# Optimization experiments

Hardware: AMD Instinct MI355X
Metric: run time of the kernel (lower is better)

## Reference

```python
import jax, jax.numpy as jnp
import numpy as np

B, C, H, W = 8, 384, 32, 32
NUM_HEADS = 8
HEAD_DIM = C // NUM_HEADS


def setup_inputs() -> dict:
    key = jax.random.key(0)
    k1, k2, k3, k4, k5 = jax.random.split(key, 5)
    s = 1.0 / np.sqrt(C)
    return {
        "x": jax.random.normal(k1, (B, C, H, W), dtype=jnp.float32),
        "w_qkv": jax.random.normal(k2, (3 * C, C), dtype=jnp.float32) * s,   # 1x1 conv == linear over channels
        "b_qkv": jax.random.normal(k3, (3 * C,), dtype=jnp.float32) * 0.01,
        "w_proj": jax.random.normal(k4, (C, C), dtype=jnp.float32) * s,
        "b_proj": jax.random.normal(k5, (C,), dtype=jnp.float32) * 0.01,
    }


def reference(x, w_qkv, b_qkv, w_proj, b_proj):
    b, c, h, w = x.shape
    n = h * w
    scale = HEAD_DIM ** (-0.5)
    # 1x1 conv qkv: (B, 3C, H, W)
    qkv = jnp.einsum('bchw,oc->bohw', x, w_qkv) + b_qkv[None, :, None, None]
    # 'b (three hd d) h0 w0 -> three b hd (h0 w0) d'
    qkv = qkv.reshape(b, 3, NUM_HEADS, HEAD_DIM, n)
    qkv = jnp.transpose(qkv, (1, 0, 2, 4, 3))  # (3, B, heads, N, d)
    q, k, v = qkv[0], qkv[1], qkv[2]
    attn = jnp.einsum('bhnd,bhmd->bhnm', q, k) * scale
    attn = jax.nn.softmax(attn, axis=-1)
    out = jnp.einsum('bhnm,bhmd->bhnd', attn, v)          # (B, heads, N, d)
    out = jnp.transpose(out, (0, 1, 3, 2)).reshape(b, c, h, w)  # b (hd d) h w
    out = jnp.einsum('bchw,oc->bohw', out, w_proj) + b_proj[None, :, None, None]
    return out
```

## Files before the change

### kernel.cpp

```cpp
#include <hip/hip_runtime.h>
#include <hip/hip_bf16.h>

typedef __hip_bfloat16 bf16;
typedef __bf16 bfx8 __attribute__((ext_vector_type(8)));
typedef float f32x4 __attribute__((ext_vector_type(4)));

#define Bk   8
#define Ck   384
#define NHk  8
#define Dk   48
#define Dp   64
#define Nk   1024
#define O3   1152


__global__ __launch_bounds__(256) void xpose_kernel(
    const float* __restrict__ x, bf16* __restrict__ Xs)
{
    __shared__ bf16 tile[32][33];
    const int b = blockIdx.z, c0 = blockIdx.y * 32, n0 = blockIdx.x * 32;
    const int tn = threadIdx.x & 31, tc = threadIdx.x >> 5;
    const float* xb = x + (size_t)b * Ck * Nk;
    #pragma unroll
    for (int i = 0; i < 4; ++i)
        tile[tc + 8 * i][tn] = __float2bfloat16(xb[(size_t)(c0 + tc + 8 * i) * Nk + n0 + tn]);
    __syncthreads();
    bf16* base = Xs + ((size_t)b * 64 + (n0 >> 4)) * 48 * 128 + (c0 >> 3) * 128;
    #pragma unroll
    for (int i = 0; i < 4; ++i) {
        int n_loc = tc + 8 * i, c_loc = tn;
        base[(size_t)(n_loc >> 4) * 6144 + (c_loc >> 3) * 128 +
             (n_loc & 15) * 8 + (c_loc & 7)] = tile[c_loc][n_loc];
    }
}

__global__ __launch_bounds__(256) void wconv_kernel(
    const float* __restrict__ wq, const float* __restrict__ wp,
    bf16* __restrict__ Wq, bf16* __restrict__ Wp,
    bf16* __restrict__ Qs, bf16* __restrict__ Ks)
{
    int i = blockIdx.x * 256 + threadIdx.x;
    if (i < O3 * Ck) {
        int o = i / Ck, c = i - o * Ck;
        Wq[((size_t)(o >> 4) * 48 + (c >> 3)) * 128 + (o & 15) * 8 + (c & 7)] =
            __float2bfloat16(wq[i]);
    }
    if (i < Ck * Ck) {
        int o = i / Ck, c = i - o * Ck;
        Wp[((size_t)(o >> 4) * 48 + (c >> 3)) * 128 + (o & 15) * 8 + (c & 7)] =
            __float2bfloat16(wp[i]);
    }
    if (i < 262144) {
        int buf = i >> 17;
        int r17 = i & 131071;
        int head = r17 >> 11;
        int r11 = r17 & 2047;
        int g = r11 >> 5, c5 = r11 & 31;
        int cd = 6 + (c5 >> 4), e = c5 & 15;
        bf16* p = (buf ? Ks : Qs) + (size_t)head * 65536 +
                  ((size_t)g * 8 + cd) * 128 + e * 8;
        *(int4*)p = (int4){0, 0, 0, 0};
    }
}

__global__ __launch_bounds__(256) void qkv_mfma_kernel(
    const bf16* __restrict__ Xs, const bf16* __restrict__ Wq,
    const float* __restrict__ bias,
    bf16* __restrict__ Qs, bf16* __restrict__ Ks, bf16* __restrict__ Vs)
{
    const int b    = blockIdx.z;
    const int by   = blockIdx.y;
    const int bx   = blockIdx.x;
    const int o0   = by * 64;
    const int n0   = bx * 128;
    const int wave = threadIdx.x >> 6;
    const int lane = threadIdx.x & 63;
    const int l15  = lane & 15, quad = lane >> 4;
    const int t3   = o0 / Ck;

    const bf16* xg[2];
    const bf16* wg[4];
    #pragma unroll
    for (int i = 0; i < 2; ++i)
        xg[i] = Xs + ((size_t)(b * 64 + bx * 8 + wave * 2 + i) * 48) * 128 + lane * 8;
    #pragma unroll
    for (int j = 0; j < 4; ++j)
        wg[j] = Wq + ((size_t)(by * 4 + j) * 48) * 128 + lane * 8;

    f32x4 acc[8];
    #pragma unroll
    for (int i = 0; i < 8; ++i) acc[i] = (f32x4){0.f, 0.f, 0.f, 0.f};

    if (t3 < 2) {
        #pragma unroll
        for (int s = 0; s < 12; ++s) {
            bfx8 fx[2], fw[4];
            #pragma unroll
            for (int i = 0; i < 2; ++i) fx[i] = *(const bfx8*)(xg[i] + s * 512);
            #pragma unroll
            for (int j = 0; j < 4; ++j) fw[j] = *(const bfx8*)(wg[j] + s * 512);
            #pragma unroll
            for (int i = 0; i < 2; ++i)
                #pragma unroll
                for (int j = 0; j < 4; ++j)
                    acc[i * 4 + j] = __builtin_amdgcn_mfma_f32_16x16x32_bf16(
                        fx[i], fw[j], acc[i * 4 + j], 0, 0, 0);
        }
        const float qscale = 0.2082350964f;
        #pragma unroll
        for (int j = 0; j < 4; ++j) {
            int o  = o0 + j * 16 + l15;
            float bi = bias[o];
            int r  = o - t3 * Ck;
            int hd = r / Dk, d = r - hd * Dk;
            bf16* hb = (t3 == 0 ? Qs : Ks) + (size_t)(b * NHk + hd) * 65536
                     + (d >> 3) * 128 + (d & 7);
            #pragma unroll
            for (int i = 0; i < 2; ++i) {
                #pragma unroll
                for (int reg = 0; reg < 4; ++reg) {
                    int npos = n0 + wave * 32 + i * 16 + quad * 4 + reg;
                    float v = acc[i * 4 + j][reg] + bi;
                    if (t3 == 0) v *= qscale;
                    hb[(size_t)(npos >> 4) * 1024 + (npos & 15) * 8] = __float2bfloat16(v);
                }
            }
        }
    } else {
        #pragma unroll
        for (int s = 0; s < 12; ++s) {
            bfx8 fx[2], fw[4];
            #pragma unroll
            for (int i = 0; i < 2; ++i) fx[i] = *(const bfx8*)(xg[i] + s * 512);
            #pragma unroll
            for (int j = 0; j < 4; ++j) fw[j] = *(const bfx8*)(wg[j] + s * 512);
            #pragma unroll
            for (int j = 0; j < 4; ++j)
                #pragma unroll
                for (int i = 0; i < 2; ++i)
                    acc[j * 2 + i] = __builtin_amdgcn_mfma_f32_16x16x32_bf16(
                        fw[j], fx[i], acc[j * 2 + i], 0, 0, 0);
        }
        #pragma unroll
        for (int j = 0; j < 4; ++j) {
            #pragma unroll
            for (int reg = 0; reg < 4; ++reg) {
                int o  = o0 + j * 16 + quad * 4 + reg;
                float bi = bias[o];
                int r  = o - 2 * Ck;
                int hd = r / Dk, d = r - hd * Dk;
                bf16* vb = Vs + (size_t)(b * NHk + hd) * 49152
                         + ((size_t)(d >> 4) * 128) * 128 + (d & 15) * 8;
                #pragma unroll
                for (int i = 0; i < 2; ++i) {
                    int npos = n0 + wave * 32 + i * 16 + l15;
                    vb[(size_t)(npos >> 3) * 128 + (npos & 7)] =
                        __float2bfloat16(acc[j * 2 + i][reg] + bi);
                }
            }
        }
    }
}

__global__ __launch_bounds__(256) void attn_kernel(
    const bf16* __restrict__ Qs, const bf16* __restrict__ Ks,
    const bf16* __restrict__ Vs, bf16* __restrict__ AO)
{
    __shared__ __align__(16) short Ps[4 * 16 * 72];
    __shared__ float sums[4][16];

    const int bx   = blockIdx.x;
    const int hd   = blockIdx.y;
    const int b    = blockIdx.z;
    const int t    = threadIdx.x;
    const int wave = t >> 6;
    const int lane = t & 63;
    const int l15  = lane & 15;
    const int quad = lane >> 4;
    const int grp  = bx * 4 + wave;

    const bf16* qb = Qs + (size_t)(b * NHk + hd) * 65536;
    const bf16* kb = Ks + (size_t)(b * NHk + hd) * 65536;
    const bf16* vb = Vs + (size_t)(b * NHk + hd) * 49152;

    const bf16* qp = qb + ((size_t)grp * 8 + quad) * 128 + l15 * 8;
    const bfx8 bq0 = *(const bfx8*)(qp);
    const bfx8 bq1 = *(const bfx8*)(qp + 512);

    float l_run = 0.f;
    f32x4 oacc[3];
    #pragma unroll
    for (int dc = 0; dc < 3; ++dc) oacc[dc] = (f32x4){0.f, 0.f, 0.f, 0.f};

    short* PsW = Ps + wave * 16 * 72;

    for (int k0 = 0; k0 < Nk; k0 += 64) {
        f32x4 sf[4];
        #pragma unroll
        for (int s = 0; s < 4; ++s) {
            const bf16* kp = kb + ((size_t)((k0 >> 4) + s) * 8 + quad) * 128 + l15 * 8;
            const bfx8 kf0 = *(const bfx8*)(kp);
            const bfx8 kf1 = *(const bfx8*)(kp + 512);
            f32x4 z = (f32x4){0.f, 0.f, 0.f, 0.f};
            z = __builtin_amdgcn_mfma_f32_16x16x32_bf16(kf0, bq0, z, 0, 0, 0);
            z = __builtin_amdgcn_mfma_f32_16x16x32_bf16(kf1, bq1, z, 0, 0, 0);
            sf[s] = z;
        }

        float lsum = 0.f;
        #pragma unroll
        for (int s = 0; s < 4; ++s) {
            ushort4 pk;
            float e0 = __builtin_amdgcn_exp2f(sf[s][0]);
            float e1 = __builtin_amdgcn_exp2f(sf[s][1]);
            float e2 = __builtin_amdgcn_exp2f(sf[s][2]);
            float e3 = __builtin_amdgcn_exp2f(sf[s][3]);
            lsum += (e0 + e1) + (e2 + e3);
            bf16 h0 = __float2bfloat16(e0), h1 = __float2bfloat16(e1);
            bf16 h2 = __float2bfloat16(e2), h3 = __float2bfloat16(e3);
            pk.x = *(unsigned short*)&h0; pk.y = *(unsigned short*)&h1;
            pk.z = *(unsigned short*)&h2; pk.w = *(unsigned short*)&h3;
            *(ushort4*)&PsW[l15 * 72 + s * 16 + quad * 4] = pk;
        }
        l_run += lsum;

        asm volatile("s_waitcnt lgkmcnt(0)" ::: "memory");

        const bfx8 ap0 = *(const bfx8*)&PsW[l15 * 72 + quad * 8];
        const bfx8 ap1 = *(const bfx8*)&PsW[l15 * 72 + 32 + quad * 8];
        #pragma unroll
        for (int dc = 0; dc < 3; ++dc) {
            const bf16* vp = vb + ((size_t)dc * 128 + (k0 >> 3) + quad) * 128 + l15 * 8;
            const bfx8 bv0 = *(const bfx8*)(vp);
            const bfx8 bv1 = *(const bfx8*)(vp + 512);
            oacc[dc] = __builtin_amdgcn_mfma_f32_16x16x32_bf16(ap0, bv0, oacc[dc], 0, 0, 0);
            oacc[dc] = __builtin_amdgcn_mfma_f32_16x16x32_bf16(ap1, bv1, oacc[dc], 0, 0, 0);
        }
    }

    {
        float lt = l_run;
        lt += __shfl_xor(lt, 16, 64);
        lt += __shfl_xor(lt, 32, 64);
        sums[wave][l15] = lt;
    }
    asm volatile("s_waitcnt lgkmcnt(0)" ::: "memory");

    short* OsW = PsW;
    #pragma unroll
    for (int r = 0; r < 4; ++r) {
        int qi = quad * 4 + r;
        float rli = 1.0f / sums[wave][qi];
        #pragma unroll
        for (int dcc = 0; dcc < 3; ++dcc) {
            bf16 hb = __float2bfloat16(oacc[dcc][r] * rli);
            OsW[qi * 64 + dcc * 16 + l15] = *(short*)&hb;
        }
    }
    asm volatile("s_waitcnt lgkmcnt(0)" ::: "memory");

    bf16* aob = AO + (((size_t)b * 64 + grp) * 48 + hd * 6) * 128;
    {
        int u = lane;
        int4 v = *(const int4*)&OsW[(u & 15) * 64 + (u >> 4) * 8];
        *(int4*)(aob + u * 8) = v;
        if (lane < 32) {
            int u2 = 64 + lane;
            int4 v2 = *(const int4*)&OsW[(u2 & 15) * 64 + (u2 >> 4) * 8];
            *(int4*)(aob + u2 * 8) = v2;
        }
    }
}

__global__ __launch_bounds__(256) void proj_mfma_kernel(
    const bf16* __restrict__ AO, const bf16* __restrict__ Wp,
    const float* __restrict__ bias, float* __restrict__ out)
{
    const int b    = blockIdx.z;
    const int by   = blockIdx.y;
    const int bx   = blockIdx.x;
    const int o0   = by * 64;
    const int n0   = bx * 128;
    const int wave = threadIdx.x >> 6;
    const int lane = threadIdx.x & 63;
    const int l15  = lane & 15, quad = lane >> 4;

    const bf16* ag[2];
    const bf16* wg[4];
    #pragma unroll
    for (int i = 0; i < 2; ++i)
        ag[i] = AO + ((size_t)(b * 64 + bx * 8 + wave * 2 + i) * 48) * 128 + lane * 8;
    #pragma unroll
    for (int j = 0; j < 4; ++j)
        wg[j] = Wp + ((size_t)(by * 4 + j) * 48) * 128 + lane * 8;

    f32x4 acc[8];
    #pragma unroll
    for (int i = 0; i < 8; ++i) acc[i] = (f32x4){0.f, 0.f, 0.f, 0.f};

    #pragma unroll
    for (int s = 0; s < 12; ++s) {
        bfx8 fx[2], fw[4];
        #pragma unroll
        for (int i = 0; i < 2; ++i) fx[i] = *(const bfx8*)(ag[i] + s * 512);
        #pragma unroll
        for (int j = 0; j < 4; ++j) fw[j] = *(const bfx8*)(wg[j] + s * 512);
        #pragma unroll
        for (int j = 0; j < 4; ++j)
            #pragma unroll
            for (int i = 0; i < 2; ++i)
                acc[j * 2 + i] = __builtin_amdgcn_mfma_f32_16x16x32_bf16(
                    fw[j], fx[i], acc[j * 2 + i], 0, 0, 0);
    }

    #pragma unroll
    for (int j = 0; j < 4; ++j) {
        #pragma unroll
        for (int reg = 0; reg < 4; ++reg) {
            int o  = o0 + j * 16 + quad * 4 + reg;
            float bi = bias[o];
            #pragma unroll
            for (int i = 0; i < 2; ++i) {
                int npos = n0 + wave * 32 + i * 16 + l15;
                out[((size_t)b * Ck + o) * Nk + npos] = acc[j * 2 + i][reg] + bi;
            }
        }
    }
}

extern "C" void kernel_launch(void* const* d_in, const int* in_sizes, int n_in,
                              void* d_out, int out_size, void* d_ws, size_t ws_size,
                              hipStream_t stream)
{
    const float* x      = (const float*)d_in[0];
    const float* w_qkv  = (const float*)d_in[1];
    const float* b_qkv  = (const float*)d_in[2];
    const float* w_proj = (const float*)d_in[3];
    const float* b_proj = (const float*)d_in[4];
    float* out = (float*)d_out;

    const size_t XT_SEG = (size_t)Bk * Nk * Ck;
    const size_t WQ_SEG = (size_t)O3 * Ck;
    const size_t WP_SEG = (size_t)Ck * Ck;
    const size_t QK_SEG = (size_t)Bk * NHk * Nk * Dp;
    const size_t V_SEG  = (size_t)Bk * NHk * Dk * Nk;

    bf16* Xs = (bf16*)d_ws;
    bf16* Wq = Xs + XT_SEG;
    bf16* Wp = Wq + WQ_SEG;
    bf16* Qs = Wp + WP_SEG;
    bf16* Ks = Qs + QK_SEG;
    bf16* Vs = Ks + QK_SEG;
    bf16* AO = Vs + V_SEG;

    xpose_kernel<<<dim3(Nk / 32, Ck / 32, Bk), 256, 0, stream>>>(x, Xs);
    wconv_kernel<<<(O3 * Ck + 255) / 256, 256, 0, stream>>>(
        w_qkv, w_proj, Wq, Wp, Qs, Ks);
    qkv_mfma_kernel<<<dim3(Nk / 128, O3 / 64, Bk), 256, 0, stream>>>(
        Xs, Wq, b_qkv, Qs, Ks, Vs);
    attn_kernel<<<dim3(16, NHk, Bk), 256, 0, stream>>>(Qs, Ks, Vs, AO);
    proj_mfma_kernel<<<dim3(Nk / 128, Ck / 64, Bk), 256, 0, stream>>>(
        AO, Wp, b_proj, out);
}
```

Measured before the change: 134.3 us.

## Stage K and V tiles in shared memory per block in attention loop

Each iteration now cooperatively loads the 64-key K tile and the matching V tile into padded LDS buffers, bracketed by two __syncthreads. The four waves then read their MFMA operands from LDS instead of each fetching the same K/V fragments from global memory. This cuts redundant global/L2 traffic four-fold, at the cost of two block-wide barriers per iteration with no double buffering, so load latency is no longer hidden behind compute.

New measurement: 135.4 us. No clear change (+0.8%).

```diff
diff --git a/kernel.cpp b/kernel.cpp
--- a/kernel.cpp
+++ b/kernel.cpp
@@ -166,6 +166,8 @@
     const bf16* __restrict__ Qs, const bf16* __restrict__ Ks,
     const bf16* __restrict__ Vs, bf16* __restrict__ AO)
 {
+    __shared__ __align__(16) short Kls[32 * 136];
+    __shared__ __align__(16) short Vls[24 * 136];
     __shared__ __align__(16) short Ps[4 * 16 * 72];
     __shared__ float sums[4][16];
 
@@ -195,12 +197,35 @@
     short* PsW = Ps + wave * 16 * 72;
 
     for (int k0 = 0; k0 < Nk; k0 += 64) {
+        __syncthreads();
+        {
+            const bf16* ksrc = kb + (size_t)(k0 >> 4) * 1024;
+            #pragma unroll
+            for (int i = 0; i < 2; ++i) {
+                int u = t + 256 * i;
+                *(bfx8*)&Kls[(u >> 4) * 136 + (u & 15) * 8] =
+                    *(const bfx8*)(ksrc + u * 8);
+            }
+            {
+                int u = t;
+                *(bfx8*)&Vls[(u >> 4) * 136 + (u & 15) * 8] =
+                    *(const bfx8*)(vb + (size_t)(u >> 7) * 16384 +
+                                   (size_t)(k0 >> 3) * 128 + (u & 127) * 8);
+                if (t < 128) {
+                    int u2 = 256 + t;
+                    *(bfx8*)&Vls[(u2 >> 4) * 136 + (u2 & 15) * 8] =
+                        *(const bfx8*)(vb + (size_t)(u2 >> 7) * 16384 +
+                                       (size_t)(k0 >> 3) * 128 + (u2 & 127) * 8);
+                }
+            }
+        }
+        __syncthreads();
+
         f32x4 sf[4];
         #pragma unroll
         for (int s = 0; s < 4; ++s) {
-            const bf16* kp = kb + ((size_t)((k0 >> 4) + s) * 8 + quad) * 128 + l15 * 8;
-            const bfx8 kf0 = *(const bfx8*)(kp);
-            const bfx8 kf1 = *(const bfx8*)(kp + 512);
+            const bfx8 kf0 = *(const bfx8*)&Kls[(s * 8 + quad) * 136 + l15 * 8];
+            const bfx8 kf1 = *(const bfx8*)&Kls[(s * 8 + quad + 4) * 136 + l15 * 8];
             f32x4 z = (f32x4){0.f, 0.f, 0.f, 0.f};
             z = __builtin_amdgcn_mfma_f32_16x16x32_bf16(kf0, bq0, z, 0, 0, 0);
             z = __builtin_amdgcn_mfma_f32_16x16x32_bf16(kf1, bq1, z, 0, 0, 0);
@@ -230,9 +255,8 @@
         const bfx8 ap1 = *(const bfx8*)&PsW[l15 * 72 + 32 + quad * 8];
         #pragma unroll
         for (int dc = 0; dc < 3; ++dc) {
-            const bf16* vp = vb + ((size_t)dc * 128 + (k0 >> 3) + quad) * 128 + l15 * 8;
-            const bfx8 bv0 = *(const bfx8*)(vp);
-            const bfx8 bv1 = *(const bfx8*)(vp + 512);
+            const bfx8 bv0 = *(const bfx8*)&Vls[(dc * 8 + quad) * 136 + l15 * 8];
+            const bfx8 bv1 = *(const bfx8*)&Vls[(dc * 8 + quad + 4) * 136 + l15 * 8];
             oacc[dc] = __builtin_amdgcn_mfma_f32_16x16x32_bf16(ap0, bv0, oacc[dc], 0, 0, 0);
             oacc[dc] = __builtin_amdgcn_mfma_f32_16x16x32_bf16(ap1, bv1, oacc[dc], 0, 0, 0);
         }
```

## Split attention over key halves and merge partials in projection; fuse prep kernels

Applied to the files above, without the earlier changes.

Attention now runs with the key range split into two halves, doubling the grid (16x8x16 blocks) to raise occupancy on the GPU. Each half writes unnormalized fp32 partial outputs and row sums, and the projection kernel merges the two halves, normalizes, and converts to bf16 while loading its A operand. The transpose and weight-conversion kernels are also merged into one launch. In exchange there is more global traffic for the fp32 partials and extra ALU work in the projection's inner loop. The merge relies on there being no running-max subtraction, since scores go straight to exp2.

Result: slower. 142.8 us (+6.3%).

```diff
diff --git a/kernel.cpp b/kernel.cpp
--- a/kernel.cpp
+++ b/kernel.cpp
@@ -14,52 +14,53 @@
 #define O3   1152
 
 
-__global__ __launch_bounds__(256) void xpose_kernel(
-    const float* __restrict__ x, bf16* __restrict__ Xs)
+__global__ __launch_bounds__(256) void prep_kernel(
+    const float* __restrict__ x, const float* __restrict__ wq,
+    const float* __restrict__ wp,
+    bf16* __restrict__ Xs, bf16* __restrict__ Wq, bf16* __restrict__ Wp,
+    bf16* __restrict__ Qs, bf16* __restrict__ Ks)
 {
     __shared__ bf16 tile[32][33];
-    const int b = blockIdx.z, c0 = blockIdx.y * 32, n0 = blockIdx.x * 32;
-    const int tn = threadIdx.x & 31, tc = threadIdx.x >> 5;
-    const float* xb = x + (size_t)b * Ck * Nk;
-    #pragma unroll
-    for (int i = 0; i < 4; ++i)
-        tile[tc + 8 * i][tn] = __float2bfloat16(xb[(size_t)(c0 + tc + 8 * i) * Nk + n0 + tn]);
-    __syncthreads();
-    bf16* base = Xs + ((size_t)b * 64 + (n0 >> 4)) * 48 * 128 + (c0 >> 3) * 128;
-    #pragma unroll
-    for (int i = 0; i < 4; ++i) {
-        int n_loc = tc + 8 * i, c_loc = tn;
-        base[(size_t)(n_loc >> 4) * 6144 + (c_loc >> 3) * 128 +
-             (n_loc & 15) * 8 + (c_loc & 7)] = tile[c_loc][n_loc];
-    }
-}
-
-__global__ __launch_bounds__(256) void wconv_kernel(
-    const float* __restrict__ wq, const float* __restrict__ wp,
-    bf16* __restrict__ Wq, bf16* __restrict__ Wp,
-    bf16* __restrict__ Qs, bf16* __restrict__ Ks)
-{
-    int i = blockIdx.x * 256 + threadIdx.x;
-    if (i < O3 * Ck) {
-        int o = i / Ck, c = i - o * Ck;
-        Wq[((size_t)(o >> 4) * 48 + (c >> 3)) * 128 + (o & 15) * 8 + (c & 7)] =
-            __float2bfloat16(wq[i]);
-    }
-    if (i < Ck * Ck) {
-        int o = i / Ck, c = i - o * Ck;
-        Wp[((size_t)(o >> 4) * 48 + (c >> 3)) * 128 + (o & 15) * 8 + (c & 7)] =
-            __float2bfloat16(wp[i]);
-    }
-    if (i < 262144) {
-        int buf = i >> 17;
-        int r17 = i & 131071;
-        int head = r17 >> 11;
-        int r11 = r17 & 2047;
-        int g = r11 >> 5, c5 = r11 & 31;
-        int cd = 6 + (c5 >> 4), e = c5 & 15;
-        bf16* p = (buf ? Ks : Qs) + (size_t)head * 65536 +
-                  ((size_t)g * 8 + cd) * 128 + e * 8;
-        *(int4*)p = (int4){0, 0, 0, 0};
+    const int bid = blockIdx.x;
+    if (bid < 3072) {
+        const int b = bid / 384, r = bid % 384;
+        const int c0 = (r / 32) * 32, n0 = (r % 32) * 32;
+        const int tn = threadIdx.x & 31, tc = threadIdx.x >> 5;
+        const float* xb = x + (size_t)b * Ck * Nk;
+        #pragma unroll
+        for (int i = 0; i < 4; ++i)
+            tile[tc + 8 * i][tn] = __float2bfloat16(xb[(size_t)(c0 + tc + 8 * i) * Nk + n0 + tn]);
+        __syncthreads();
+        bf16* base = Xs + ((size_t)b * 64 + (n0 >> 4)) * 48 * 128 + (c0 >> 3) * 128;
+        #pragma unroll
+        for (int i = 0; i < 4; ++i) {
+            int n_loc = tc + 8 * i, c_loc = tn;
+            base[(size_t)(n_loc >> 4) * 6144 + (c_loc >> 3) * 128 +
+                 (n_loc & 15) * 8 + (c_loc & 7)] = tile[c_loc][n_loc];
+        }
+    } else {
+        int i = (bid - 3072) * 256 + threadIdx.x;
+        if (i < O3 * Ck) {
+            int o = i / Ck, c = i - o * Ck;
+            Wq[((size_t)(o >> 4) * 48 + (c >> 3)) * 128 + (o & 15) * 8 + (c & 7)] =
+                __float2bfloat16(wq[i]);
+        }
+        if (i < Ck * Ck) {
+            int o = i / Ck, c = i - o * Ck;
+            Wp[((size_t)(o >> 4) * 48 + (c >> 3)) * 128 + (o & 15) * 8 + (c & 7)] =
+                __float2bfloat16(wp[i]);
+        }
+        if (i < 262144) {
+            int buf = i >> 17;
+            int r17 = i & 131071;
+            int head = r17 >> 11;
+            int r11 = r17 & 2047;
+            int g = r11 >> 5, c5 = r11 & 31;
+            int cd = 6 + (c5 >> 4), e = c5 & 15;
+            bf16* p = (buf ? Ks : Qs) + (size_t)head * 65536 +
+                      ((size_t)g * 8 + cd) * 128 + e * 8;
+            *(int4*)p = (int4){0, 0, 0, 0};
+        }
     }
 }
 
@@ -164,14 +165,15 @@
 
 __global__ __launch_bounds__(256) void attn_kernel(
     const bf16* __restrict__ Qs, const bf16* __restrict__ Ks,
-    const bf16* __restrict__ Vs, bf16* __restrict__ AO)
+    const bf16* __restrict__ Vs, float* __restrict__ Op, float* __restrict__ Lp)
 {
     __shared__ __align__(16) short Ps[4 * 16 * 72];
-    __shared__ float sums[4][16];
 
     const int bx   = blockIdx.x;
     const int hd   = blockIdx.y;
-    const int b    = blockIdx.z;
+    const int bz   = blockIdx.z;
+    const int b    = bz >> 1;
+    const int half = bz & 1;
     const int t    = threadIdx.x;
     const int wave = t >> 6;
     const int lane = t & 63;
@@ -194,7 +196,8 @@
 
     short* PsW = Ps + wave * 16 * 72;
 
-    for (int k0 = 0; k0 < Nk; k0 += 64) {
+    const int kbeg = half * 512;
+    for (int k0 = kbeg; k0 < kbeg + 512; k0 += 64) {
         f32x4 sf[4];
         #pragma unroll
         for (int s = 0; s < 4; ++s) {
@@ -242,39 +245,26 @@
         float lt = l_run;
         lt += __shfl_xor(lt, 16, 64);
         lt += __shfl_xor(lt, 32, 64);
-        sums[wave][l15] = lt;
-    }
-    asm volatile("s_waitcnt lgkmcnt(0)" ::: "memory");
-
-    short* OsW = PsW;
+        if (lane < 16)
+            Lp[((size_t)(half * 8 + b) * 8 + hd) * 1024 + grp * 16 + lane] = lt;
+    }
+
+    float* opb = Op + (((size_t)(half * 512) + b * 64 + grp) * 48 + hd * 6) * 128;
     #pragma unroll
     for (int r = 0; r < 4; ++r) {
-        int qi = quad * 4 + r;
-        float rli = 1.0f / sums[wave][qi];
+        int row = quad * 4 + r;
         #pragma unroll
         for (int dcc = 0; dcc < 3; ++dcc) {
-            bf16 hb = __float2bfloat16(oacc[dcc][r] * rli);
-            OsW[qi * 64 + dcc * 16 + l15] = *(short*)&hb;
-        }
-    }
-    asm volatile("s_waitcnt lgkmcnt(0)" ::: "memory");
-
-    bf16* aob = AO + (((size_t)b * 64 + grp) * 48 + hd * 6) * 128;
-    {
-        int u = lane;
-        int4 v = *(const int4*)&OsW[(u & 15) * 64 + (u >> 4) * 8];
-        *(int4*)(aob + u * 8) = v;
-        if (lane < 32) {
-            int u2 = 64 + lane;
-            int4 v2 = *(const int4*)&OsW[(u2 & 15) * 64 + (u2 >> 4) * 8];
-            *(int4*)(aob + u2 * 8) = v2;
+            int d = dcc * 16 + l15;
+            opb[(d >> 3) * 128 + row * 8 + (d & 7)] = oacc[dcc][r];
         }
     }
 }
 
 __global__ __launch_bounds__(256) void proj_mfma_kernel(
-    const bf16* __restrict__ AO, const bf16* __restrict__ Wp,
-    const float* __restrict__ bias, float* __restrict__ out)
+    const float* __restrict__ Op, const float* __restrict__ Lp,
+    const bf16* __restrict__ Wp, const float* __restrict__ bias,
+    float* __restrict__ out)
 {
     const int b    = blockIdx.z;
     const int by   = blockIdx.y;
@@ -285,11 +275,17 @@
     const int lane = threadIdx.x & 63;
     const int l15  = lane & 15, quad = lane >> 4;
 
-    const bf16* ag[2];
+    const size_t HOFF = (size_t)512 * 48 * 128;
+
+    const float* og[2];
+    int nrow[2];
+    #pragma unroll
+    for (int i = 0; i < 2; ++i) {
+        int gi = bx * 8 + wave * 2 + i;
+        og[i]   = Op + ((size_t)(b * 64 + gi) * 48) * 128 + lane * 8;
+        nrow[i] = gi * 16 + l15;
+    }
     const bf16* wg[4];
-    #pragma unroll
-    for (int i = 0; i < 2; ++i)
-        ag[i] = AO + ((size_t)(b * 64 + bx * 8 + wave * 2 + i) * 48) * 128 + lane * 8;
     #pragma unroll
     for (int j = 0; j < 4; ++j)
         wg[j] = Wp + ((size_t)(by * 4 + j) * 48) * 128 + lane * 8;
@@ -300,11 +296,33 @@
 
     #pragma unroll
     for (int s = 0; s < 12; ++s) {
-        bfx8 fx[2], fw[4];
-        #pragma unroll
-        for (int i = 0; i < 2; ++i) fx[i] = *(const bfx8*)(ag[i] + s * 512);
+        bfx8 fw[4];
         #pragma unroll
         for (int j = 0; j < 4; ++j) fw[j] = *(const bfx8*)(wg[j] + s * 512);
+
+        const int hdq = (s * 4 + quad) / 6;
+        bfx8 fx[2];
+        #pragma unroll
+        for (int i = 0; i < 2; ++i) {
+            const float* p = og[i] + s * 512;
+            float4 a0 = *(const float4*)(p);
+            float4 a1 = *(const float4*)(p + 4);
+            float4 c0 = *(const float4*)(p + HOFF);
+            float4 c1 = *(const float4*)(p + HOFF + 4);
+            float l1 = Lp[((size_t)b * 8 + hdq) * 1024 + nrow[i]];
+            float l2 = Lp[((size_t)(8 + b) * 8 + hdq) * 1024 + nrow[i]];
+            float rli = 1.0f / (l1 + l2);
+            bfx8 af;
+            af[0] = (__bf16)((a0.x + c0.x) * rli);
+            af[1] = (__bf16)((a0.y + c0.y) * rli);
+            af[2] = (__bf16)((a0.z + c0.z) * rli);
+            af[3] = (__bf16)((a0.w + c0.w) * rli);
+            af[4] = (__bf16)((a1.x + c1.x) * rli);
+            af[5] = (__bf16)((a1.y + c1.y) * rli);
+            af[6] = (__bf16)((a1.z + c1.z) * rli);
+            af[7] = (__bf16)((a1.w + c1.w) * rli);
+            fx[i] = af;
+        }
         #pragma unroll
         for (int j = 0; j < 4; ++j)
             #pragma unroll
@@ -344,6 +362,7 @@
     const size_t WP_SEG = (size_t)Ck * Ck;
     const size_t QK_SEG = (size_t)Bk * NHk * Nk * Dp;
     const size_t V_SEG  = (size_t)Bk * NHk * Dk * Nk;
+    const size_t OP_SEG = (size_t)2 * Bk * 64 * 48 * 128;
 
     bf16* Xs = (bf16*)d_ws;
     bf16* Wq = Xs + XT_SEG;
@@ -351,14 +370,13 @@
     bf16* Qs = Wp + WP_SEG;
     bf16* Ks = Qs + QK_SEG;
     bf16* Vs = Ks + QK_SEG;
-    bf16* AO = Vs + V_SEG;
-
-    xpose_kernel<<<dim3(Nk / 32, Ck / 32, Bk), 256, 0, stream>>>(x, Xs);
-    wconv_kernel<<<(O3 * Ck + 255) / 256, 256, 0, stream>>>(
-        w_qkv, w_proj, Wq, Wp, Qs, Ks);
+    float* Op = (float*)(Vs + V_SEG);
+    float* Lp = Op + OP_SEG;
+
+    prep_kernel<<<4800, 256, 0, stream>>>(x, w_qkv, w_proj, Xs, Wq, Wp, Qs, Ks);
     qkv_mfma_kernel<<<dim3(Nk / 128, O3 / 64, Bk), 256, 0, stream>>>(
         Xs, Wq, b_qkv, Qs, Ks, Vs);
-    attn_kernel<<<dim3(16, NHk, Bk), 256, 0, stream>>>(Qs, Ks, Vs, AO);
+    attn_kernel<<<dim3(16, NHk, Bk * 2), 256, 0, stream>>>(Qs, Ks, Vs, Op, Lp);
     proj_mfma_kernel<<<dim3(Nk / 128, Ck / 64, Bk), 256, 0, stream>>>(
-        AO, Wp, b_proj, out);
-}
+        Op, Lp, Wp, b_proj, out);
+}
```

## Merge prep kernels and double-buffer K loads in attention loop

Applied to the files above, without the earlier changes.

Fuses the x transpose and weight-conversion kernels into one launch, removing a kernel launch boundary. In the attention kernel, the K fragments for the next 64-key tile are prefetched into registers while the current tile runs, and V loads are issued early. A launch-bounds occupancy hint of 4 blocks is also added. This raises register pressure, which may cap occupancy or cause spills.

Result: slower. 146.3 us (+8.9%).

```diff
diff --git a/kernel.cpp b/kernel.cpp
--- a/kernel.cpp
+++ b/kernel.cpp
@@ -14,52 +14,53 @@
 #define O3   1152
 
 
-__global__ __launch_bounds__(256) void xpose_kernel(
-    const float* __restrict__ x, bf16* __restrict__ Xs)
+__global__ __launch_bounds__(256) void prep_kernel(
+    const float* __restrict__ x, const float* __restrict__ wq,
+    const float* __restrict__ wp,
+    bf16* __restrict__ Xs, bf16* __restrict__ Wq, bf16* __restrict__ Wp,
+    bf16* __restrict__ Qs, bf16* __restrict__ Ks)
 {
     __shared__ bf16 tile[32][33];
-    const int b = blockIdx.z, c0 = blockIdx.y * 32, n0 = blockIdx.x * 32;
-    const int tn = threadIdx.x & 31, tc = threadIdx.x >> 5;
-    const float* xb = x + (size_t)b * Ck * Nk;
-    #pragma unroll
-    for (int i = 0; i < 4; ++i)
-        tile[tc + 8 * i][tn] = __float2bfloat16(xb[(size_t)(c0 + tc + 8 * i) * Nk + n0 + tn]);
-    __syncthreads();
-    bf16* base = Xs + ((size_t)b * 64 + (n0 >> 4)) * 48 * 128 + (c0 >> 3) * 128;
-    #pragma unroll
-    for (int i = 0; i < 4; ++i) {
-        int n_loc = tc + 8 * i, c_loc = tn;
-        base[(size_t)(n_loc >> 4) * 6144 + (c_loc >> 3) * 128 +
-             (n_loc & 15) * 8 + (c_loc & 7)] = tile[c_loc][n_loc];
-    }
-}
-
-__global__ __launch_bounds__(256) void wconv_kernel(
-    const float* __restrict__ wq, const float* __restrict__ wp,
-    bf16* __restrict__ Wq, bf16* __restrict__ Wp,
-    bf16* __restrict__ Qs, bf16* __restrict__ Ks)
-{
-    int i = blockIdx.x * 256 + threadIdx.x;
-    if (i < O3 * Ck) {
-        int o = i / Ck, c = i - o * Ck;
-        Wq[((size_t)(o >> 4) * 48 + (c >> 3)) * 128 + (o & 15) * 8 + (c & 7)] =
-            __float2bfloat16(wq[i]);
-    }
-    if (i < Ck * Ck) {
-        int o = i / Ck, c = i - o * Ck;
-        Wp[((size_t)(o >> 4) * 48 + (c >> 3)) * 128 + (o & 15) * 8 + (c & 7)] =
-            __float2bfloat16(wp[i]);
-    }
-    if (i < 262144) {
-        int buf = i >> 17;
-        int r17 = i & 131071;
-        int head = r17 >> 11;
-        int r11 = r17 & 2047;
-        int g = r11 >> 5, c5 = r11 & 31;
-        int cd = 6 + (c5 >> 4), e = c5 & 15;
-        bf16* p = (buf ? Ks : Qs) + (size_t)head * 65536 +
-                  ((size_t)g * 8 + cd) * 128 + e * 8;
-        *(int4*)p = (int4){0, 0, 0, 0};
+    const int bid = blockIdx.x;
+    if (bid < 3072) {
+        const int b = bid / 384, r = bid % 384;
+        const int c0 = (r / 32) * 32, n0 = (r % 32) * 32;
+        const int tn = threadIdx.x & 31, tc = threadIdx.x >> 5;
+        const float* xb = x + (size_t)b * Ck * Nk;
+        #pragma unroll
+        for (int i = 0; i < 4; ++i)
+            tile[tc + 8 * i][tn] = __float2bfloat16(xb[(size_t)(c0 + tc + 8 * i) * Nk + n0 + tn]);
+        __syncthreads();
+        bf16* base = Xs + ((size_t)b * 64 + (n0 >> 4)) * 48 * 128 + (c0 >> 3) * 128;
+        #pragma unroll
+        for (int i = 0; i < 4; ++i) {
+            int n_loc = tc + 8 * i, c_loc = tn;
+            base[(size_t)(n_loc >> 4) * 6144 + (c_loc >> 3) * 128 +
+                 (n_loc & 15) * 8 + (c_loc & 7)] = tile[c_loc][n_loc];
+        }
+    } else {
+        int i = (bid - 3072) * 256 + threadIdx.x;
+        if (i < O3 * Ck) {
+            int o = i / Ck, c = i - o * Ck;
+            Wq[((size_t)(o >> 4) * 48 + (c >> 3)) * 128 + (o & 15) * 8 + (c & 7)] =
+                __float2bfloat16(wq[i]);
+        }
+        if (i < Ck * Ck) {
+            int o = i / Ck, c = i - o * Ck;
+            Wp[((size_t)(o >> 4) * 48 + (c >> 3)) * 128 + (o & 15) * 8 + (c & 7)] =
+                __float2bfloat16(wp[i]);
+        }
+        if (i < 262144) {
+            int buf = i >> 17;
+            int r17 = i & 131071;
+            int head = r17 >> 11;
+            int r11 = r17 & 2047;
+            int g = r11 >> 5, c5 = r11 & 31;
+            int cd = 6 + (c5 >> 4), e = c5 & 15;
+            bf16* p = (buf ? Ks : Qs) + (size_t)head * 65536 +
+                      ((size_t)g * 8 + cd) * 128 + e * 8;
+            *(int4*)p = (int4){0, 0, 0, 0};
+        }
     }
 }
 
@@ -162,7 +163,7 @@
     }
 }
 
-__global__ __launch_bounds__(256) void attn_kernel(
+__global__ __launch_bounds__(256, 4) void attn_kernel(
     const bf16* __restrict__ Qs, const bf16* __restrict__ Ks,
     const bf16* __restrict__ Vs, bf16* __restrict__ AO)
 {
@@ -193,50 +194,68 @@
     for (int dc = 0; dc < 3; ++dc) oacc[dc] = (f32x4){0.f, 0.f, 0.f, 0.f};
 
     short* PsW = Ps + wave * 16 * 72;
-
-    for (int k0 = 0; k0 < Nk; k0 += 64) {
-        f32x4 sf[4];
-        #pragma unroll
-        for (int s = 0; s < 4; ++s) {
-            const bf16* kp = kb + ((size_t)((k0 >> 4) + s) * 8 + quad) * 128 + l15 * 8;
-            const bfx8 kf0 = *(const bfx8*)(kp);
-            const bfx8 kf1 = *(const bfx8*)(kp + 512);
-            f32x4 z = (f32x4){0.f, 0.f, 0.f, 0.f};
-            z = __builtin_amdgcn_mfma_f32_16x16x32_bf16(kf0, bq0, z, 0, 0, 0);
-            z = __builtin_amdgcn_mfma_f32_16x16x32_bf16(kf1, bq1, z, 0, 0, 0);
-            sf[s] = z;
-        }
-
-        float lsum = 0.f;
-        #pragma unroll
-        for (int s = 0; s < 4; ++s) {
-            ushort4 pk;
-            float e0 = __builtin_amdgcn_exp2f(sf[s][0]);
-            float e1 = __builtin_amdgcn_exp2f(sf[s][1]);
-            float e2 = __builtin_amdgcn_exp2f(sf[s][2]);
-            float e3 = __builtin_amdgcn_exp2f(sf[s][3]);
-            lsum += (e0 + e1) + (e2 + e3);
-            bf16 h0 = __float2bfloat16(e0), h1 = __float2bfloat16(e1);
-            bf16 h2 = __float2bfloat16(e2), h3 = __float2bfloat16(e3);
-            pk.x = *(unsigned short*)&h0; pk.y = *(unsigned short*)&h1;
-            pk.z = *(unsigned short*)&h2; pk.w = *(unsigned short*)&h3;
-            *(ushort4*)&PsW[l15 * 72 + s * 16 + quad * 4] = pk;
-        }
-        l_run += lsum;
-
-        asm volatile("s_waitcnt lgkmcnt(0)" ::: "memory");
-
-        const bfx8 ap0 = *(const bfx8*)&PsW[l15 * 72 + quad * 8];
-        const bfx8 ap1 = *(const bfx8*)&PsW[l15 * 72 + 32 + quad * 8];
-        #pragma unroll
-        for (int dc = 0; dc < 3; ++dc) {
-            const bf16* vp = vb + ((size_t)dc * 128 + (k0 >> 3) + quad) * 128 + l15 * 8;
-            const bfx8 bv0 = *(const bfx8*)(vp);
-            const bfx8 bv1 = *(const bfx8*)(vp + 512);
-            oacc[dc] = __builtin_amdgcn_mfma_f32_16x16x32_bf16(ap0, bv0, oacc[dc], 0, 0, 0);
-            oacc[dc] = __builtin_amdgcn_mfma_f32_16x16x32_bf16(ap1, bv1, oacc[dc], 0, 0, 0);
-        }
-    }
+    const bf16* kbase = kb + (size_t)quad * 128 + l15 * 8;
+    const bf16* vbase = vb + (size_t)quad * 128 + l15 * 8;
+
+    bfx8 kA[8], kB[8];
+
+#define LOADK(dst, k0)                                                        \
+    {                                                                         \
+        _Pragma("unroll")                                                     \
+        for (int s = 0; s < 4; ++s) {                                         \
+            const bf16* kp = kbase + (size_t)((k0 >> 4) + s) * 1024;          \
+            dst[s * 2]     = *(const bfx8*)kp;                                \
+            dst[s * 2 + 1] = *(const bfx8*)(kp + 512);                        \
+        }                                                                     \
+    }
+
+#define TILE(kcur, knxt, k0, PF)                                              \
+    {                                                                         \
+        bfx8 vv[6];                                                           \
+        _Pragma("unroll")                                                     \
+        for (int dc = 0; dc < 3; ++dc) {                                      \
+            const bf16* vp = vbase + (size_t)dc * 16384 + ((k0) >> 3) * 128;  \
+            vv[dc * 2]     = *(const bfx8*)vp;                                \
+            vv[dc * 2 + 1] = *(const bfx8*)(vp + 512);                        \
+        }                                                                     \
+        float lsum = 0.f;                                                     \
+        _Pragma("unroll")                                                     \
+        for (int s = 0; s < 4; ++s) {                                         \
+            f32x4 z = (f32x4){0.f, 0.f, 0.f, 0.f};                            \
+            z = __builtin_amdgcn_mfma_f32_16x16x32_bf16(kcur[s * 2], bq0, z, 0, 0, 0); \
+            z = __builtin_amdgcn_mfma_f32_16x16x32_bf16(kcur[s * 2 + 1], bq1, z, 0, 0, 0); \
+            float e0 = __builtin_amdgcn_exp2f(z[0]);                          \
+            float e1 = __builtin_amdgcn_exp2f(z[1]);                          \
+            float e2 = __builtin_amdgcn_exp2f(z[2]);                          \
+            float e3 = __builtin_amdgcn_exp2f(z[3]);                          \
+            lsum += (e0 + e1) + (e2 + e3);                                    \
+            bf16 h0 = __float2bfloat16(e0), h1 = __float2bfloat16(e1);        \
+            bf16 h2 = __float2bfloat16(e2), h3 = __float2bfloat16(e3);        \
+            ushort4 pk;                                                       \
+            pk.x = *(unsigned short*)&h0; pk.y = *(unsigned short*)&h1;       \
+            pk.z = *(unsigned short*)&h2; pk.w = *(unsigned short*)&h3;       \
+            *(ushort4*)&PsW[l15 * 72 + s * 16 + quad * 4] = pk;               \
+        }                                                                     \
+        l_run += lsum;                                                        \
+        if (PF) LOADK(knxt, (k0) + 64)                                        \
+        asm volatile("s_waitcnt lgkmcnt(0)" ::: "memory");                    \
+        const bfx8 ap0 = *(const bfx8*)&PsW[l15 * 72 + quad * 8];             \
+        const bfx8 ap1 = *(const bfx8*)&PsW[l15 * 72 + 32 + quad * 8];        \
+        _Pragma("unroll")                                                     \
+        for (int dc = 0; dc < 3; ++dc) {                                      \
+            oacc[dc] = __builtin_amdgcn_mfma_f32_16x16x32_bf16(ap0, vv[dc * 2], oacc[dc], 0, 0, 0); \
+            oacc[dc] = __builtin_amdgcn_mfma_f32_16x16x32_bf16(ap1, vv[dc * 2 + 1], oacc[dc], 0, 0, 0); \
+        }                                                                     \
+    }
+
+    LOADK(kA, 0)
+    for (int tt = 0; tt < 8; ++tt) {
+        const int k0 = tt * 128;
+        TILE(kA, kB, k0, 1)
+        TILE(kB, kA, k0 + 64, (tt < 7))
+    }
+#undef TILE
+#undef LOADK
 
     {
         float lt = l_run;
@@ -353,9 +372,7 @@
     bf16* Vs = Ks + QK_SEG;
     bf16* AO = Vs + V_SEG;
 
-    xpose_kernel<<<dim3(Nk / 32, Ck / 32, Bk), 256, 0, stream>>>(x, Xs);
-    wconv_kernel<<<(O3 * Ck + 255) / 256, 256, 0, stream>>>(
-        w_qkv, w_proj, Wq, Wp, Qs, Ks);
+    prep_kernel<<<4800, 256, 0, stream>>>(x, w_qkv, w_proj, Xs, Wq, Wp, Qs, Ks);
     qkv_mfma_kernel<<<dim3(Nk / 128, O3 / 64, Bk), 256, 0, stream>>>(
         Xs, Wq, b_qkv, Qs, Ks, Vs);
     attn_kernel<<<dim3(16, NHk, Bk), 256, 0, stream>>>(Qs, Ks, Vs, AO);
```
